# Optimization experiments

Measured on AMD Instinct MI355X. Metric: run time of the kernel, lower is better.

The kernel has to match this reference:

```python
import jax, jax.numpy as jnp
import numpy as np

B, T, C, HS = 8, 2048, 768, 256  # batch, seq(block_size), n_embed, head_size


def setup_inputs() -> dict:
    key = jax.random.key(0)
    kx, kq, kk, kv = jax.random.split(key, 4)
    scale = 1.0 / np.sqrt(C)
    return {
        "x": jax.random.normal(kx, (B, T, C), dtype=jnp.float32),
        # torch nn.Linear(n_embed, head_size, bias=False) computes x @ W.T;
        # store weights pre-transposed as [in, out].
        "Wq": jax.random.normal(kq, (C, HS), dtype=jnp.float32) * scale,
        "Wk": jax.random.normal(kk, (C, HS), dtype=jnp.float32) * scale,
        "Wv": jax.random.normal(kv, (C, HS), dtype=jnp.float32) * scale,
    }


def reference(x, Wq, Wk, Wv):
    Bx, Tx, Cx = x.shape
    q = x @ Wq  # [B,T,HS]
    k = x @ Wk  # [B,T,HS]
    v = x @ Wv  # [B,T,HS]
    # NOTE: original scales by C**-0.5 with C = n_embed (not head_size)
    att = jnp.einsum('btd,bsd->bts', q, k) * (Cx ** -0.5)  # [B,T,T]
    causal = jnp.tril(jnp.ones((Tx, Tx), dtype=bool))
    att = jnp.where(causal, att, -jnp.inf)
    probs = jax.nn.softmax(att, axis=-1)
    # dropout=0.0 -> identity (eval mode)
    out = jnp.einsum('bts,bsd->btd', probs, v)  # [B,T,HS]
    return out
```

## Files before the change

kernel.cpp:

```cpp
#include <hip/hip_runtime.h>
#include <hip/hip_bf16.h>
#include <math.h>

#define B_  8
#define T_  2048
#define C_  768
#define HS_ 256

#define CHUNKS_PER_BATCH 144
#define NSLOT (CHUNKS_PER_BATCH * B_)

typedef float  f32x4  __attribute__((ext_vector_type(4)));
typedef __bf16 bf16x8 __attribute__((ext_vector_type(8)));
typedef __bf16 bf16x4 __attribute__((ext_vector_type(4)));
typedef __bf16 bf16x2 __attribute__((ext_vector_type(2)));

#define MFMA16(a, b, c) __builtin_amdgcn_mfma_f32_16x16x32_bf16((a), (b), (c), 0, 0, 0)

#define GLOAD_LDS16(gp, lp)                                                     \
    __builtin_amdgcn_global_load_lds(                                           \
        (const __attribute__((address_space(1))) void*)(gp),                    \
        (__attribute__((address_space(3))) void*)(lp), 16, 0, 0)

__device__ __forceinline__ int chunk_cum64(int qb) {
    int g = qb >> 2;
    return 2 * g * (g + 1) + (qb & 3) * (g + 1);
}

__global__ __launch_bounds__(256) void prep_kernel(const float* __restrict__ x,
                                                   const float* __restrict__ Wq,
                                                   const float* __restrict__ Wk,
                                                   const float* __restrict__ Wv,
                                                   __bf16* __restrict__ xb,
                                                   __bf16* __restrict__ wt_all,
                                                   float qscale) {
    const int bid = blockIdx.x;
    if (bid < 6144) {
        size_t i = ((size_t)bid * 256 + threadIdx.x) * 8;
        f32x4 a = *(const f32x4*)(x + i);
        f32x4 b = *(const f32x4*)(x + i + 4);
        bf16x8 o;
        o[0] = (__bf16)a[0]; o[1] = (__bf16)a[1]; o[2] = (__bf16)a[2]; o[3] = (__bf16)a[3];
        o[4] = (__bf16)b[0]; o[5] = (__bf16)b[1]; o[6] = (__bf16)b[2]; o[7] = (__bf16)b[3];
        *(bf16x8*)(xb + i) = o;
    } else {
        int idx = (bid - 6144) * 256 + threadIdx.x;
        int n   = idx & 255;
        int t   = idx >> 8;
        int mat = t / 96;
        int k8  = t - mat * 96;
        const float* W = (mat == 0) ? Wq : ((mat == 1) ? Wk : Wv);
        float scale = (mat == 0) ? qscale : 1.0f;
        bf16x8 o;
#pragma unroll
        for (int j = 0; j < 8; j++)
            o[j] = (__bf16)(W[(k8 * 8 + j) * HS_ + n] * scale);
        *(bf16x8*)&wt_all[((size_t)mat * HS_ + n) * C_ + k8 * 8] = o;
    }
}

__global__ __launch_bounds__(256) void proj_kernel(const __bf16* __restrict__ xb,
                                                   const __bf16* __restrict__ wt,
                                                   __bf16* __restrict__ qf_,
                                                   __bf16* __restrict__ kf_,
                                                   __bf16* __restrict__ vf_) {
    __shared__ alignas(16) __bf16 ldsA[2][128 * 32];
    __shared__ alignas(16) __bf16 ldsB[2][128 * 32];

    const int tid  = threadIdx.x;
    const int w    = tid >> 6;
    const int lane = tid & 63;
    const int cm   = lane & 15;
    const int quad = lane >> 4;
    const int wm   = w & 1;
    const int wn   = w >> 1;
    const int m0   = blockIdx.x * 128;
    const int n0   = blockIdx.y * 128;
    const int mat  = n0 >> 8;

    f32x4 acc[4][4];
#pragma unroll
    for (int i = 0; i < 4; i++)
#pragma unroll
        for (int j = 0; j < 4; j++) acc[i][j] = (f32x4){0.f, 0.f, 0.f, 0.f};

#pragma unroll
    for (int h = 0; h < 2; h++) {
        int c = tid + h * 256;
        GLOAD_LDS16(xb + (size_t)(m0 + (c >> 2)) * C_ + (c & 3) * 8, &ldsA[0][c * 8]);
        GLOAD_LDS16(wt + (size_t)(n0 + (c >> 2)) * C_ + (c & 3) * 8, &ldsB[0][c * 8]);
    }

    for (int kt = 0; kt < 24; kt++) {
        const int cur = kt & 1;
        __syncthreads();

        if (kt < 23) {
            const int k0 = (kt + 1) * 32;
#pragma unroll
            for (int h = 0; h < 2; h++) {
                int c = tid + h * 256;
                GLOAD_LDS16(xb + (size_t)(m0 + (c >> 2)) * C_ + k0 + (c & 3) * 8,
                            &ldsA[cur ^ 1][c * 8]);
                GLOAD_LDS16(wt + (size_t)(n0 + (c >> 2)) * C_ + k0 + (c & 3) * 8,
                            &ldsB[cur ^ 1][c * 8]);
            }
        }

        bf16x8 af[4], bfr[4];
#pragma unroll
        for (int mt = 0; mt < 4; mt++)
            af[mt] = *(const bf16x8*)&ldsA[cur][(wm * 64 + mt * 16 + cm) * 32 + quad * 8];
#pragma unroll
        for (int nt = 0; nt < 4; nt++)
            bfr[nt] = *(const bf16x8*)&ldsB[cur][(wn * 64 + nt * 16 + cm) * 32 + quad * 8];
        if (mat < 2) {
#pragma unroll
            for (int dt = 0; dt < 4; dt++)
#pragma unroll
                for (int qt2 = 0; qt2 < 4; qt2++)
                    acc[dt][qt2] = MFMA16(bfr[dt], af[qt2], acc[dt][qt2]);
        } else {
#pragma unroll
            for (int mt = 0; mt < 4; mt++)
#pragma unroll
                for (int nt = 0; nt < 4; nt++)
                    acc[mt][nt] = MFMA16(af[mt], bfr[nt], acc[mt][nt]);
        }
    }

    const int dBase = (n0 & 255) + wn * 64;
    const int b     = m0 >> 11;
    if (mat < 2) {
        const int rt2 = ((m0 & 2047) >> 6) + wm;
        __bf16* dst = (mat == 0) ? qf_ : kf_;
#pragma unroll
        for (int dt = 0; dt < 4; dt++)
#pragma unroll
            for (int qt2 = 0; qt2 < 4; qt2++) {
                int d0    = dBase + dt * 16 + quad * 4;
                int ksq   = d0 >> 5;
                int quadp = (d0 >> 3) & 3;
                int j0    = d0 & 7;
                size_t addr;
                if (mat == 0)
                    addr = ((((size_t)(b * 32 + rt2) * 4 + qt2) * 8 + ksq) * 64
                            + quadp * 16 + cm) * 8 + j0;
                else
                    addr = ((((size_t)(b * 32 + rt2) * 8 + ksq) * 4 + qt2) * 64
                            + quadp * 16 + cm) * 8 + j0;
                bf16x4 v4;
                v4[0] = (__bf16)acc[dt][qt2][0]; v4[1] = (__bf16)acc[dt][qt2][1];
                v4[2] = (__bf16)acc[dt][qt2][2]; v4[3] = (__bf16)acc[dt][qt2][3];
                *(bf16x4*)(dst + addr) = v4;
            }
    } else {
        const int rt = ((m0 & 2047) + wm * 64) >> 6;
#pragma unroll
        for (int mt = 0; mt < 4; mt++) {
            int ks2   = (mt >> 1) & 1;
            int quadF = (mt & 1) * 2 + (quad >> 1);
            int jb    = (quad & 1) * 4;
#pragma unroll
            for (int nt = 0; nt < 4; nt++) {
                int ntv = (dBase >> 4) + nt;
                size_t idx = ((((size_t)(b * 32 + rt) * 2 + ks2) * 16 + ntv) * 64
                              + quadF * 16 + cm) * 8 + jb;
                bf16x4 v4;
                v4[0] = (__bf16)acc[mt][nt][0]; v4[1] = (__bf16)acc[mt][nt][1];
                v4[2] = (__bf16)acc[mt][nt][2]; v4[3] = (__bf16)acc[mt][nt][3];
                *(bf16x4*)(vf_ + idx) = v4;
            }
        }
    }
}

__global__ __launch_bounds__(256, 2) void flash_part(const __bf16* __restrict__ qf_,
                                                     const __bf16* __restrict__ kf_,
                                                     const __bf16* __restrict__ vf_,
                                                     __bf16* __restrict__ Opart,
                                                     float* __restrict__ mpart,
                                                     float* __restrict__ lpart) {
    __shared__ alignas(16) __bf16 ldsK[2][8 * 2 * 64 * 8];
    __shared__ alignas(16) __bf16 ldsV[2][16 * 64 * 8];
    __shared__ alignas(16) __bf16 ldsP[4][512];

    const int tid  = threadIdx.x;
    const int w    = tid >> 6;
    const int lane = tid & 63;
    const int cm   = lane & 15;
    const int quad = lane >> 4;

    const int pid  = blockIdx.x;
    const int b    = pid & 7;
    const int r    = (CHUNKS_PER_BATCH - 1) - (pid >> 3);
    int qb = 0, ci = 0;
    {
        int rr = r;
        for (int j = 0; j < 32; j++) {
            int c = (j >> 2) + 1;
            if (rr < c) { qb = j; ci = rr; break; }
            rr -= c;
        }
    }
    const int lpid = b * CHUNKS_PER_BATCH + r;
    const int kt_begin = ci * 8;
    const int kt_end   = min(kt_begin + 8, 2 * qb + 2);

    const __bf16* qp = qf_ + (((size_t)(b * 32 + qb) * 4 + w) * 8) * 512 + lane * 8;
    bf16x8 qf[8];
#pragma unroll
    for (int ks = 0; ks < 8; ks++) qf[ks] = *(const bf16x8*)(qp + ks * 512);

    auto stage = [&](int bsel, int kt) {
        const int kt64 = kt >> 1, kh = kt & 1;
        const __bf16* kgb = kf_ + (((size_t)(b * 32 + kt64) * 8) * 4 + kh * 2) * 512;
#pragma unroll
        for (int h = 0; h < 4; h++) {
            int g = h * 256 + tid;
            int ks = g >> 7, sub = g & 127;
            GLOAD_LDS16(kgb + (size_t)ks * 4 * 512 + sub * 8,
                        &ldsK[bsel][(h * 256 + w * 64) * 8]);
        }
        const __bf16* vgb = vf_ + ((size_t)(b * 64 + kt) * 16) * 512;
#pragma unroll
        for (int h = 0; h < 4; h++) {
            int g = h * 256 + tid;
            GLOAD_LDS16(vgb + (size_t)g * 8,
                        &ldsV[bsel][(h * 256 + w * 64) * 8]);
        }
    };

    f32x4 accO[16];
#pragma unroll
    for (int i = 0; i < 16; i++) accO[i] = (f32x4){0.f, 0.f, 0.f, 0.f};
    float mi = 0.f, li = 0.f;

    const int wrow  = qb * 64 + w * 16;
    const int qglob = wrow + cm;

    stage(0, kt_begin);
    asm volatile("s_waitcnt vmcnt(0)" ::: "memory");
    __builtin_amdgcn_s_barrier();

    int cur = 0;
    for (int kt = kt_begin; kt < kt_end; kt++) {
        if (kt + 1 < kt_end) stage(cur ^ 1, kt + 1);

        f32x4 s[2];
#pragma unroll
        for (int i = 0; i < 2; i++) s[i] = (f32x4){0.f, 0.f, 0.f, 0.f};
        __builtin_amdgcn_s_setprio(1);
#pragma unroll
        for (int ns = 0; ns < 2; ns++)
#pragma unroll
            for (int ks = 0; ks < 8; ks++) {
                bf16x8 kfr = *(const bf16x8*)&ldsK[cur][(ks * 2 + ns) * 512 + lane * 8];
                s[ns] = MFMA16(kfr, qf[ks], s[ns]);
            }
        __builtin_amdgcn_s_setprio(0);
        if (kt * 32 + 31 > wrow) {
#pragma unroll
            for (int ns = 0; ns < 2; ns++)
#pragma unroll
                for (int i = 0; i < 4; i++)
                    if (kt * 32 + ns * 16 + quad * 4 + i > qglob)
                        s[ns][i] = -__builtin_inff();
        }
        if (kt == kt_begin) {
            float pm = -__builtin_inff();
#pragma unroll
            for (int ns = 0; ns < 2; ns++)
#pragma unroll
                for (int i = 0; i < 4; i++) pm = fmaxf(pm, s[ns][i]);
            pm = fmaxf(pm, __shfl_xor(pm, 16));
            pm = fmaxf(pm, __shfl_xor(pm, 32));
            mi = pm;
        }
        float p[2][4], rs = 0.f;
#pragma unroll
        for (int ns = 0; ns < 2; ns++)
#pragma unroll
            for (int i = 0; i < 4; i++) {
                p[ns][i] = exp2f(s[ns][i] - mi);
                rs += p[ns][i];
            }
        rs += __shfl_xor(rs, 16);
        rs += __shfl_xor(rs, 32);
        li += rs;

#pragma unroll
        for (int ns = 0; ns < 2; ns++)
#pragma unroll
            for (int i2 = 0; i2 < 2; i2++) {
                bf16x2 d2;
                d2[0] = (__bf16)p[ns][2 * i2];
                d2[1] = (__bf16)p[ns][2 * i2 + 1];
                int off = ((ns * 2 + (quad >> 1)) * 16 + cm) * 8
                          + (quad & 1) * 4 + i2 * 2;
                *(bf16x2*)&ldsP[w][off] = d2;
            }
        bf16x8 pfrag = *(const bf16x8*)&ldsP[w][(quad * 16 + cm) * 8];
        __builtin_amdgcn_s_setprio(1);
#pragma unroll
        for (int nt = 0; nt < 16; nt++) {
            bf16x8 vfr = *(const bf16x8*)&ldsV[cur][(nt * 64 + lane) * 8];
            accO[nt] = MFMA16(vfr, pfrag, accO[nt]);
        }
        __builtin_amdgcn_s_setprio(0);

        asm volatile("s_waitcnt vmcnt(0)" ::: "memory");
        __builtin_amdgcn_s_barrier();
        cur ^= 1;
    }

    __bf16* op = Opart + ((size_t)lpid * 64 + w * 16 + cm) * HS_;
#pragma unroll
    for (int nt = 0; nt < 16; nt++) {
        bf16x4 v4;
        v4[0] = (__bf16)accO[nt][0]; v4[1] = (__bf16)accO[nt][1];
        v4[2] = (__bf16)accO[nt][2]; v4[3] = (__bf16)accO[nt][3];
        *(bf16x4*)(op + nt * 16 + quad * 4) = v4;
    }
    if (quad == 0) {
        mpart[lpid * 64 + w * 16 + cm] = mi;
        lpart[lpid * 64 + w * 16 + cm] = li;
    }
}

__global__ __launch_bounds__(256) void flash_combine(const __bf16* __restrict__ Opart,
                                                     const float* __restrict__ mpart,
                                                     const float* __restrict__ lpart,
                                                     float* __restrict__ out) {
    const int b    = blockIdx.x >> 5;
    const int qb   = blockIdx.x & 31;
    const int nc   = (qb >> 2) + 1;
    const int pid0 = b * CHUNKS_PER_BATCH + chunk_cum64(qb);

    const int tid  = threadIdx.x;
    const int col  = (tid & 63) * 4;
    const int r0   = blockIdx.y * 16 + (tid >> 6) * 4;

    f32x4 ms = (f32x4){-__builtin_inff(), -__builtin_inff(),
                       -__builtin_inff(), -__builtin_inff()};
    for (int c = 0; c < nc; c++) {
        f32x4 m4 = *(const f32x4*)(mpart + (pid0 + c) * 64 + r0);
#pragma unroll
        for (int i = 0; i < 4; i++) ms[i] = fmaxf(ms[i], m4[i]);
    }
    f32x4 acc[4];
#pragma unroll
    for (int i = 0; i < 4; i++) acc[i] = (f32x4){0.f, 0.f, 0.f, 0.f};
    f32x4 lt = (f32x4){0.f, 0.f, 0.f, 0.f};
    for (int c = 0; c < nc; c++) {
        f32x4 m4 = *(const f32x4*)(mpart + (pid0 + c) * 64 + r0);
        f32x4 l4 = *(const f32x4*)(lpart + (pid0 + c) * 64 + r0);
#pragma unroll
        for (int i = 0; i < 4; i++) {
            float sc = exp2f(m4[i] - ms[i]);
            lt[i] += l4[i] * sc;
            bf16x4 o = *(const bf16x4*)(Opart
                        + ((size_t)(pid0 + c) * 64 + r0 + i) * HS_ + col);
            acc[i][0] += (float)o[0] * sc; acc[i][1] += (float)o[1] * sc;
            acc[i][2] += (float)o[2] * sc; acc[i][3] += (float)o[3] * sc;
        }
    }
#pragma unroll
    for (int i = 0; i < 4; i++) {
        float inv = 1.0f / lt[i];
        f32x4 res = (f32x4){acc[i][0] * inv, acc[i][1] * inv,
                            acc[i][2] * inv, acc[i][3] * inv};
        *(f32x4*)(out + ((size_t)(b * T_ + qb * 64 + r0 + i)) * HS_ + col) = res;
    }
}

extern "C" void kernel_launch(void* const* d_in, const int* in_sizes, int n_in,
                              void* d_out, int out_size, void* d_ws, size_t ws_size,
                              hipStream_t stream) {
    const float* x  = (const float*)d_in[0];
    const float* Wq = (const float*)d_in[1];
    const float* Wk = (const float*)d_in[2];
    const float* Wv = (const float*)d_in[3];
    float* out = (float*)d_out;

    char* ws = (char*)d_ws;
    size_t off = 0;
    __bf16* wt_all = (__bf16*)(ws + off); off += 1179648;
    __bf16* qfrag  = (__bf16*)(ws + off); off += 8388608;
    __bf16* kfrag  = (__bf16*)(ws + off); off += 8388608;
    __bf16* vfrag  = (__bf16*)(ws + off); off += 8388608;
    __bf16* xb     = (__bf16*)(ws + off);
    __bf16* Opart  = (__bf16*)(ws + off); off += (size_t)NSLOT * 64 * HS_ * 2;
    float*  mpart  = (float*)(ws + off);  off += (size_t)NSLOT * 64 * 4;
    float*  lpart  = (float*)(ws + off);

    float qscale = 1.4426950408889634f / sqrtf((float)C_);

    prep_kernel<<<dim3(6432), 256, 0, stream>>>(x, Wq, Wk, Wv, xb, wt_all, qscale);
    proj_kernel<<<dim3(128, 6), 256, 0, stream>>>(xb, wt_all, qfrag, kfrag, vfrag);
    flash_part<<<dim3(NSLOT), 256, 0, stream>>>(qfrag, kfrag, vfrag, Opart, mpart, lpart);
    flash_combine<<<dim3(256, 4), 256, 0, stream>>>(Opart, mpart, lpart, out);
}
```

Baseline: 184.6 us.

## Enlarge flash query tile to 128 rows so each K/V tile serves two query groups

Each wave now handles two 16-row query groups, so the query block per workgroup grows from 64 to 128 rows and the partition count per batch drops from 144 to 72. Each staged K/V tile in LDS feeds twice as many MFMAs, which halves K/V global traffic and LDS fragment reads per unit of work. The combine kernel and the workspace indexing are updated to match. The cost is doubled accumulator registers (accO grows to 32 vectors) under launch_bounds(256,2), which risks spills or lower occupancy, and fewer blocks in the grid.

```diff
diff --git a/kernel.cpp b/kernel.cpp
--- a/kernel.cpp
+++ b/kernel.cpp
@@ -7,7 +7,7 @@
 #define C_  768
 #define HS_ 256
 
-#define CHUNKS_PER_BATCH 144
+#define CHUNKS_PER_BATCH 72
 #define NSLOT (CHUNKS_PER_BATCH * B_)
 
 typedef float  f32x4  __attribute__((ext_vector_type(4)));
@@ -22,9 +22,9 @@
         (const __attribute__((address_space(1))) void*)(gp),                    \
         (__attribute__((address_space(3))) void*)(lp), 16, 0, 0)
 
-__device__ __forceinline__ int chunk_cum64(int qb) {
-    int g = qb >> 2;
-    return 2 * g * (g + 1) + (qb & 3) * (g + 1);
+__device__ __forceinline__ int chunk_cum128(int qb) {
+    int g = qb >> 1;
+    return g * (g + 1) + (qb & 1) * (g + 1);
 }
 
 __global__ __launch_bounds__(256) void prep_kernel(const float* __restrict__ x,
@@ -183,7 +183,7 @@
                                                      float* __restrict__ lpart) {
     __shared__ alignas(16) __bf16 ldsK[2][8 * 2 * 64 * 8];
     __shared__ alignas(16) __bf16 ldsV[2][16 * 64 * 8];
-    __shared__ alignas(16) __bf16 ldsP[4][512];
+    __shared__ alignas(16) __bf16 ldsP[4][2][512];
 
     const int tid  = threadIdx.x;
     const int w    = tid >> 6;
@@ -197,20 +197,25 @@
     int qb = 0, ci = 0;
     {
         int rr = r;
-        for (int j = 0; j < 32; j++) {
-            int c = (j >> 2) + 1;
+        for (int j = 0; j < 16; j++) {
+            int c = (j >> 1) + 1;
             if (rr < c) { qb = j; ci = rr; break; }
             rr -= c;
         }
     }
     const int lpid = b * CHUNKS_PER_BATCH + r;
     const int kt_begin = ci * 8;
-    const int kt_end   = min(kt_begin + 8, 2 * qb + 2);
-
-    const __bf16* qp = qf_ + (((size_t)(b * 32 + qb) * 4 + w) * 8) * 512 + lane * 8;
-    bf16x8 qf[8];
-#pragma unroll
-    for (int ks = 0; ks < 8; ks++) qf[ks] = *(const bf16x8*)(qp + ks * 512);
+    const int kt_end   = min(kt_begin + 8, 4 * qb + 4);
+
+    bf16x8 qf2[2][8];
+#pragma unroll
+    for (int qg = 0; qg < 2; qg++) {
+        int g16 = qb * 8 + w * 2 + qg;
+        const __bf16* qp = qf_ + (((size_t)(b * 32 + (g16 >> 2)) * 4 + (g16 & 3)) * 8) * 512
+                           + lane * 8;
+#pragma unroll
+        for (int ks = 0; ks < 8; ks++) qf2[qg][ks] = *(const bf16x8*)(qp + ks * 512);
+    }
 
     auto stage = [&](int bsel, int kt) {
         const int kt64 = kt >> 1, kh = kt & 1;
@@ -231,13 +236,14 @@
         }
     };
 
-    f32x4 accO[16];
-#pragma unroll
-    for (int i = 0; i < 16; i++) accO[i] = (f32x4){0.f, 0.f, 0.f, 0.f};
-    float mi = 0.f, li = 0.f;
-
-    const int wrow  = qb * 64 + w * 16;
-    const int qglob = wrow + cm;
+    f32x4 accO[2][16];
+#pragma unroll
+    for (int qg = 0; qg < 2; qg++)
+#pragma unroll
+        for (int i = 0; i < 16; i++) accO[qg][i] = (f32x4){0.f, 0.f, 0.f, 0.f};
+    float mi[2] = {0.f, 0.f}, li[2] = {0.f, 0.f};
+
+    const int wrow = qb * 128 + w * 32;
 
     stage(0, kt_begin);
     asm volatile("s_waitcnt vmcnt(0)" ::: "memory");
@@ -247,65 +253,85 @@
     for (int kt = kt_begin; kt < kt_end; kt++) {
         if (kt + 1 < kt_end) stage(cur ^ 1, kt + 1);
 
-        f32x4 s[2];
-#pragma unroll
-        for (int i = 0; i < 2; i++) s[i] = (f32x4){0.f, 0.f, 0.f, 0.f};
+        f32x4 s[2][2];
+#pragma unroll
+        for (int ns = 0; ns < 2; ns++)
+#pragma unroll
+            for (int qg = 0; qg < 2; qg++) s[ns][qg] = (f32x4){0.f, 0.f, 0.f, 0.f};
         __builtin_amdgcn_s_setprio(1);
 #pragma unroll
         for (int ns = 0; ns < 2; ns++)
 #pragma unroll
             for (int ks = 0; ks < 8; ks++) {
                 bf16x8 kfr = *(const bf16x8*)&ldsK[cur][(ks * 2 + ns) * 512 + lane * 8];
-                s[ns] = MFMA16(kfr, qf[ks], s[ns]);
+                s[ns][0] = MFMA16(kfr, qf2[0][ks], s[ns][0]);
+                s[ns][1] = MFMA16(kfr, qf2[1][ks], s[ns][1]);
             }
         __builtin_amdgcn_s_setprio(0);
         if (kt * 32 + 31 > wrow) {
 #pragma unroll
+            for (int qg = 0; qg < 2; qg++) {
+                int qglob = wrow + qg * 16 + cm;
+#pragma unroll
+                for (int ns = 0; ns < 2; ns++)
+#pragma unroll
+                    for (int i = 0; i < 4; i++)
+                        if (kt * 32 + ns * 16 + quad * 4 + i > qglob)
+                            s[ns][qg][i] = -__builtin_inff();
+            }
+        }
+        if (kt == kt_begin) {
+#pragma unroll
+            for (int qg = 0; qg < 2; qg++) {
+                float pm = -__builtin_inff();
+#pragma unroll
+                for (int ns = 0; ns < 2; ns++)
+#pragma unroll
+                    for (int i = 0; i < 4; i++) pm = fmaxf(pm, s[ns][qg][i]);
+                pm = fmaxf(pm, __shfl_xor(pm, 16));
+                pm = fmaxf(pm, __shfl_xor(pm, 32));
+                mi[qg] = pm;
+            }
+        }
+        float p[2][2][4];
+        float rs[2] = {0.f, 0.f};
+#pragma unroll
+        for (int qg = 0; qg < 2; qg++)
+#pragma unroll
             for (int ns = 0; ns < 2; ns++)
 #pragma unroll
-                for (int i = 0; i < 4; i++)
-                    if (kt * 32 + ns * 16 + quad * 4 + i > qglob)
-                        s[ns][i] = -__builtin_inff();
-        }
-        if (kt == kt_begin) {
-            float pm = -__builtin_inff();
+                for (int i = 0; i < 4; i++) {
+                    p[qg][ns][i] = exp2f(s[ns][qg][i] - mi[qg]);
+                    rs[qg] += p[qg][ns][i];
+                }
+#pragma unroll
+        for (int qg = 0; qg < 2; qg++) {
+            rs[qg] += __shfl_xor(rs[qg], 16);
+            rs[qg] += __shfl_xor(rs[qg], 32);
+            li[qg] += rs[qg];
+        }
+
+#pragma unroll
+        for (int qg = 0; qg < 2; qg++)
 #pragma unroll
             for (int ns = 0; ns < 2; ns++)
 #pragma unroll
-                for (int i = 0; i < 4; i++) pm = fmaxf(pm, s[ns][i]);
-            pm = fmaxf(pm, __shfl_xor(pm, 16));
-            pm = fmaxf(pm, __shfl_xor(pm, 32));
-            mi = pm;
-        }
-        float p[2][4], rs = 0.f;
-#pragma unroll
-        for (int ns = 0; ns < 2; ns++)
-#pragma unroll
-            for (int i = 0; i < 4; i++) {
-                p[ns][i] = exp2f(s[ns][i] - mi);
-                rs += p[ns][i];
-            }
-        rs += __shfl_xor(rs, 16);
-        rs += __shfl_xor(rs, 32);
-        li += rs;
-
-#pragma unroll
-        for (int ns = 0; ns < 2; ns++)
-#pragma unroll
-            for (int i2 = 0; i2 < 2; i2++) {
-                bf16x2 d2;
-                d2[0] = (__bf16)p[ns][2 * i2];
-                d2[1] = (__bf16)p[ns][2 * i2 + 1];
-                int off = ((ns * 2 + (quad >> 1)) * 16 + cm) * 8
-                          + (quad & 1) * 4 + i2 * 2;
-                *(bf16x2*)&ldsP[w][off] = d2;
-            }
-        bf16x8 pfrag = *(const bf16x8*)&ldsP[w][(quad * 16 + cm) * 8];
+                for (int i2 = 0; i2 < 2; i2++) {
+                    bf16x2 d2;
+                    d2[0] = (__bf16)p[qg][ns][2 * i2];
+                    d2[1] = (__bf16)p[qg][ns][2 * i2 + 1];
+                    int off = ((ns * 2 + (quad >> 1)) * 16 + cm) * 8
+                              + (quad & 1) * 4 + i2 * 2;
+                    *(bf16x2*)&ldsP[w][qg][off] = d2;
+                }
+        bf16x8 pf0 = *(const bf16x8*)&ldsP[w][0][(quad * 16 + cm) * 8];
+        bf16x8 pf1 = *(const bf16x8*)&ldsP[w][1][(quad * 16 + cm) * 8];
         __builtin_amdgcn_s_setprio(1);
 #pragma unroll
         for (int nt = 0; nt < 16; nt++) {
             bf16x8 vfr = *(const bf16x8*)&ldsV[cur][(nt * 64 + lane) * 8];
-            accO[nt] = MFMA16(vfr, pfrag, accO[nt]);
+            accO[0][nt] = MFMA16(vfr, pf0, accO[0][nt]);
+            accO[1][nt] = MFMA16(vfr, pf1, accO[1][nt]);
         }
         __builtin_amdgcn_s_setprio(0);
 
@@ -314,17 +340,20 @@
         cur ^= 1;
     }
 
-    __bf16* op = Opart + ((size_t)lpid * 64 + w * 16 + cm) * HS_;
-#pragma unroll
-    for (int nt = 0; nt < 16; nt++) {
-        bf16x4 v4;
-        v4[0] = (__bf16)accO[nt][0]; v4[1] = (__bf16)accO[nt][1];
-        v4[2] = (__bf16)accO[nt][2]; v4[3] = (__bf16)accO[nt][3];
-        *(bf16x4*)(op + nt * 16 + quad * 4) = v4;
-    }
-    if (quad == 0) {
-        mpart[lpid * 64 + w * 16 + cm] = mi;
-        lpart[lpid * 64 + w * 16 + cm] = li;
+#pragma unroll
+    for (int qg = 0; qg < 2; qg++) {
+        __bf16* op = Opart + ((size_t)lpid * 128 + w * 32 + qg * 16 + cm) * HS_;
+#pragma unroll
+        for (int nt = 0; nt < 16; nt++) {
+            bf16x4 v4;
+            v4[0] = (__bf16)accO[qg][nt][0]; v4[1] = (__bf16)accO[qg][nt][1];
+            v4[2] = (__bf16)accO[qg][nt][2]; v4[3] = (__bf16)accO[qg][nt][3];
+            *(bf16x4*)(op + nt * 16 + quad * 4) = v4;
+        }
+        if (quad == 0) {
+            mpart[lpid * 128 + w * 32 + qg * 16 + cm] = mi[qg];
+            lpart[lpid * 128 + w * 32 + qg * 16 + cm] = li[qg];
+        }
     }
 }
 
@@ -332,10 +361,10 @@
                                                      const float* __restrict__ mpart,
                                                      const float* __restrict__ lpart,
                                                      float* __restrict__ out) {
-    const int b    = blockIdx.x >> 5;
-    const int qb   = blockIdx.x & 31;
-    const int nc   = (qb >> 2) + 1;
-    const int pid0 = b * CHUNKS_PER_BATCH + chunk_cum64(qb);
+    const int b    = blockIdx.x >> 4;
+    const int qb   = blockIdx.x & 15;
+    const int nc   = (qb >> 1) + 1;
+    const int pid0 = b * CHUNKS_PER_BATCH + chunk_cum128(qb);
 
     const int tid  = threadIdx.x;
     const int col  = (tid & 63) * 4;
@@ -344,7 +373,7 @@
     f32x4 ms = (f32x4){-__builtin_inff(), -__builtin_inff(),
                        -__builtin_inff(), -__builtin_inff()};
     for (int c = 0; c < nc; c++) {
-        f32x4 m4 = *(const f32x4*)(mpart + (pid0 + c) * 64 + r0);
+        f32x4 m4 = *(const f32x4*)(mpart + (pid0 + c) * 128 + r0);
 #pragma unroll
         for (int i = 0; i < 4; i++) ms[i] = fmaxf(ms[i], m4[i]);
     }
@@ -353,14 +382,14 @@
     for (int i = 0; i < 4; i++) acc[i] = (f32x4){0.f, 0.f, 0.f, 0.f};
     f32x4 lt = (f32x4){0.f, 0.f, 0.f, 0.f};
     for (int c = 0; c < nc; c++) {
-        f32x4 m4 = *(const f32x4*)(mpart + (pid0 + c) * 64 + r0);
-        f32x4 l4 = *(const f32x4*)(lpart + (pid0 + c) * 64 + r0);
+        f32x4 m4 = *(const f32x4*)(mpart + (pid0 + c) * 128 + r0);
+        f32x4 l4 = *(const f32x4*)(lpart + (pid0 + c) * 128 + r0);
 #pragma unroll
         for (int i = 0; i < 4; i++) {
             float sc = exp2f(m4[i] - ms[i]);
             lt[i] += l4[i] * sc;
             bf16x4 o = *(const bf16x4*)(Opart
-                        + ((size_t)(pid0 + c) * 64 + r0 + i) * HS_ + col);
+                        + ((size_t)(pid0 + c) * 128 + r0 + i) * HS_ + col);
             acc[i][0] += (float)o[0] * sc; acc[i][1] += (float)o[1] * sc;
             acc[i][2] += (float)o[2] * sc; acc[i][3] += (float)o[3] * sc;
         }
@@ -370,7 +399,7 @@
         float inv = 1.0f / lt[i];
         f32x4 res = (f32x4){acc[i][0] * inv, acc[i][1] * inv,
                             acc[i][2] * inv, acc[i][3] * inv};
-        *(f32x4*)(out + ((size_t)(b * T_ + qb * 64 + r0 + i)) * HS_ + col) = res;
+        *(f32x4*)(out + ((size_t)(b * T_ + qb * 128 + r0 + i)) * HS_ + col) = res;
     }
 }
 
@@ -390,8 +419,8 @@
     __bf16* kfrag  = (__bf16*)(ws + off); off += 8388608;
     __bf16* vfrag  = (__bf16*)(ws + off); off += 8388608;
     __bf16* xb     = (__bf16*)(ws + off);
-    __bf16* Opart  = (__bf16*)(ws + off); off += (size_t)NSLOT * 64 * HS_ * 2;
-    float*  mpart  = (float*)(ws + off);  off += (size_t)NSLOT * 64 * 4;
+    __bf16* Opart  = (__bf16*)(ws + off); off += (size_t)NSLOT * 128 * HS_ * 2;
+    float*  mpart  = (float*)(ws + off);  off += (size_t)NSLOT * 128 * 4;
     float*  lpart  = (float*)(ws + off);
 
     float qscale = 1.4426950408889634f / sqrtf((float)C_);
@@ -399,5 +428,5 @@
     prep_kernel<<<dim3(6432), 256, 0, stream>>>(x, Wq, Wk, Wv, xb, wt_all, qscale);
     proj_kernel<<<dim3(128, 6), 256, 0, stream>>>(xb, wt_all, qfrag, kfrag, vfrag);
     flash_part<<<dim3(NSLOT), 256, 0, stream>>>(qfrag, kfrag, vfrag, Opart, mpart, lpart);
-    flash_combine<<<dim3(256, 4), 256, 0, stream>>>(Opart, mpart, lpart, out);
-}
+    flash_combine<<<dim3(128, 8), 256, 0, stream>>>(Opart, mpart, lpart, out);
+}
```

After: 187.6 us. About the same (+1.6%).
